# Performance work log

Measured on AMD Instinct MI355X. Metric: run time of the kernel, lower is better.

## Reference

```python
import jax, jax.numpy as jnp
import numpy as np

D_MODEL = 128
D_STATE = 64
EXPAND = 2
D_INNER = EXPAND * D_MODEL  # 256
D_CONV = 4
DT_RANK = (D_MODEL + 15) // 16  # 8
EPS = 1e-6


def setup_inputs() -> dict:
    key = jax.random.key(0)
    ks = jax.random.split(key, 10)
    B, L = 8, 4096
    s = lambda *sh: 1.0 / np.sqrt(sh[-1])
    inp = {
        "x": jax.random.normal(ks[0], (B, L, D_MODEL), jnp.float32),
        "norm_w": jnp.ones((D_MODEL,), jnp.float32),
        "norm_b": jnp.zeros((D_MODEL,), jnp.float32),
        "in_proj_w": jax.random.normal(ks[1], (2 * D_INNER, D_MODEL), jnp.float32) * s(D_MODEL),
        "conv_w": jax.random.normal(ks[2], (D_INNER, 1, D_CONV), jnp.float32) * 0.5,
        "conv_b": jax.random.normal(ks[3], (D_INNER,), jnp.float32) * 0.02,
        "x_proj_w": jax.random.normal(ks[4], (DT_RANK + 2 * D_STATE, D_INNER), jnp.float32) * s(D_INNER),
        "dt_proj_w": jax.random.normal(ks[5], (D_INNER, DT_RANK), jnp.float32) * s(DT_RANK),
        "dt_proj_b": jax.random.uniform(ks[6], (D_INNER,), jnp.float32, -4.0, -2.0),  # softplus -> small dt
        "A_log": jnp.log(jnp.broadcast_to(jnp.arange(1.0, D_STATE + 1.0, dtype=jnp.float32), (D_INNER, D_STATE))),
        "D": jnp.ones((D_INNER,), jnp.float32),
        "out_proj_w": jax.random.normal(ks[7], (D_MODEL, D_INNER), jnp.float32) * s(D_INNER),
    }
    return inp


def _mamba_block(x, norm_w, norm_b, in_proj_w, conv_w, conv_b, x_proj_w,
                 dt_proj_w, dt_proj_b, A_log, Dp, out_proj_w):
    B, L, _ = x.shape
    # LayerNorm (eps=1e-6)
    mu = jnp.mean(x, -1, keepdims=True)
    var = jnp.mean(jnp.square(x - mu), -1, keepdims=True)
    h = (x - mu) * jax.lax.rsqrt(var + EPS) * norm_w + norm_b
    # in_proj -> (u, z), each (B, L, d_inner)
    xz = jnp.einsum('bld,ed->ble', h, in_proj_w)
    u, z = jnp.split(xz, 2, axis=-1)
    # causal depthwise conv1d over L, then SiLU
    u_nch = jnp.transpose(u, (0, 2, 1))  # (B, d_inner, L)
    u_conv = jax.lax.conv_general_dilated(
        u_nch, conv_w, window_strides=(1,), padding=[(D_CONV - 1, 0)],
        feature_group_count=D_INNER, dimension_numbers=('NCH', 'OIH', 'NCH'))
    u_conv = jax.nn.silu(u_conv + conv_b[None, :, None])
    u = jnp.transpose(u_conv, (0, 2, 1))  # (B, L, d_inner)
    # x_proj -> dt, Bmat, Cmat
    x_dbl = jnp.einsum('bld,ed->ble', u, x_proj_w)
    dt, Bmat, Cmat = jnp.split(x_dbl, [DT_RANK, DT_RANK + D_STATE], axis=-1)
    delta = jax.nn.softplus(jnp.einsum('blr,dr->bld', dt, dt_proj_w) + dt_proj_b)  # (B,L,d_inner)
    A = -jnp.exp(A_log)  # (d_inner, d_state)
    # selective scan over L: state (B, d_inner, d_state)
    def step(hS, inp):
        d_t, B_t, C_t, u_t = inp  # (B,dI),(B,N),(B,N),(B,dI)
        dA = jnp.exp(d_t[:, :, None] * A)                      # (B,dI,N)
        hS = dA * hS + (d_t * u_t)[:, :, None] * B_t[:, None, :]
        y = jnp.einsum('bdn,bn->bd', hS, C_t)
        return hS, y
    xs = (jnp.transpose(delta, (1, 0, 2)), jnp.transpose(Bmat, (1, 0, 2)),
          jnp.transpose(Cmat, (1, 0, 2)), jnp.transpose(u, (1, 0, 2)))
    h0 = jnp.zeros((B, D_INNER, D_STATE), x.dtype)
    _, ys = jax.lax.scan(step, h0, xs)
    y = jnp.transpose(ys, (1, 0, 2)) + u * Dp  # (B,L,d_inner)
    y = y * jax.nn.silu(z)
    out = jnp.einsum('bld,ed->ble', y, out_proj_w)  # (B,L,d_model)
    return x + out  # residual (drop_path=0)


def reference(x, norm_w, norm_b, in_proj_w, conv_w, conv_b, x_proj_w,
              dt_proj_w, dt_proj_b, A_log, D, out_proj_w):
    return _mamba_block(x, norm_w, norm_b, in_proj_w, conv_w, conv_b, x_proj_w,
                        dt_proj_w, dt_proj_b, A_log, D, out_proj_w)
```

## Files before the change

kernel.cpp:

```cpp
#include <hip/hip_runtime.h>
#include <math.h>

#define DM 128
#define DI 256
#define DSN 64
#define NB 8
#define LSEQ 4096
#define NTOK (NB*LSEQ)
#define GRP 8
#define GLEN (LSEQ/GRP)

typedef float4 f4;
typedef __attribute__((ext_vector_type(8))) short bf16x8;
typedef __attribute__((ext_vector_type(4))) float f32x4;
typedef __attribute__((ext_vector_type(8))) unsigned short us8;

#if __has_builtin(__builtin_amdgcn_exp2f)
#define EXP2(x) __builtin_amdgcn_exp2f(x)
#else
#define EXP2(x) __expf((x)*0.6931471805599453f)
#endif

__device__ __forceinline__ float sigmoidf_(float x){ return 1.f/(1.f+__expf(-x)); }
__device__ __forceinline__ float rdlane(float v, int j){
    return __int_as_float(__builtin_amdgcn_readlane(__float_as_int(v), j));
}
__device__ __forceinline__ unsigned short f2bf(float f){
    unsigned u = __float_as_uint(f);
    unsigned r = u + 0x7FFFu + ((u>>16)&1u);
    return (unsigned short)(r>>16);
}

__global__ void __launch_bounds__(256) k_lnstats(const float* __restrict__ x, float* __restrict__ stats){
    int tok = blockIdx.x*4 + (threadIdx.x>>6);
    int lane = threadIdx.x & 63;
    const float* row = x + (size_t)tok*DM;
    float a = row[lane], b = row[lane+64];
    float s = a+b, ss = a*a+b*b;
    #pragma unroll
    for (int off=32; off>0; off>>=1){ s += __shfl_xor(s,off); ss += __shfl_xor(ss,off); }
    if (lane==0){
        float mu = s*(1.f/128.f);
        float var = ss*(1.f/128.f) - mu*mu;
        stats[tok*2+0] = mu;
        stats[tok*2+1] = rsqrtf(var + 1e-6f);
    }
}

template<int N_DIM,int K_DIM,int MODE>
__global__ void __launch_bounds__(256) k_gemm_bf(const float* __restrict__ Af32,
    const unsigned short* __restrict__ Abf, const float* __restrict__ Bw,
    float* __restrict__ Cout, float* __restrict__ Cout2, int ldC,
    const float* __restrict__ stats, const float* __restrict__ nw,
    const float* __restrict__ nb, const float* __restrict__ resid)
{
    __shared__ unsigned short Abuf[128*72];
    __shared__ unsigned short Bbuf[64*72];
    const int tid = threadIdx.x;
    const int m0 = blockIdx.x*128;
    const int n0 = blockIdx.y*64;
    const int wave = tid>>6, lane = tid&63;
    const int wm = wave>>1, wn = wave&1;
    const int lr = lane&15, lk = (lane>>4)*8;
    f32x4 acc[4][2];
    #pragma unroll
    for (int i=0;i<4;++i){
        #pragma unroll
        for (int j=0;j<2;++j) acc[i][j] = (f32x4){0.f,0.f,0.f,0.f};
    }

    for (int k0=0; k0<K_DIM; k0+=64){
        {
            int row = tid>>1, ks = (tid&1)*32;
            int m = m0 + row;
            unsigned short* dst = &Abuf[row*72 + ks];
            if (MODE==2){
                const unsigned short* src = Abf + (size_t)m*K_DIM + k0 + ks;
                #pragma unroll
                for (int q=0;q<4;++q) *(us8*)(dst+q*8) = *(const us8*)(src+q*8);
            } else {
                const float* src = Af32 + (size_t)m*K_DIM + k0 + ks;
                float mu=0.f, rs=1.f;
                if (MODE==0){ mu = stats[2*m]; rs = stats[2*m+1]; }
                #pragma unroll
                for (int q=0;q<4;++q){
                    f4 v0 = *(const f4*)(src+q*8);
                    f4 v1 = *(const f4*)(src+q*8+4);
                    if (MODE==0){
                        int kk = k0+ks+q*8;
                        f4 w0=*(const f4*)(nw+kk), w1=*(const f4*)(nw+kk+4);
                        f4 c0=*(const f4*)(nb+kk), c1=*(const f4*)(nb+kk+4);
                        v0.x=(v0.x-mu)*rs*w0.x+c0.x; v0.y=(v0.y-mu)*rs*w0.y+c0.y;
                        v0.z=(v0.z-mu)*rs*w0.z+c0.z; v0.w=(v0.w-mu)*rs*w0.w+c0.w;
                        v1.x=(v1.x-mu)*rs*w1.x+c1.x; v1.y=(v1.y-mu)*rs*w1.y+c1.y;
                        v1.z=(v1.z-mu)*rs*w1.z+c1.z; v1.w=(v1.w-mu)*rs*w1.w+c1.w;
                    }
                    us8 o = {f2bf(v0.x),f2bf(v0.y),f2bf(v0.z),f2bf(v0.w),
                             f2bf(v1.x),f2bf(v1.y),f2bf(v1.z),f2bf(v1.w)};
                    *(us8*)(dst+q*8) = o;
                }
            }
        }
        {
            int row = tid>>2, ks = (tid&3)*16;
            int n = n0 + row;
            unsigned short* dst = &Bbuf[row*72 + ks];
            #pragma unroll
            for (int q=0;q<2;++q){
                f4 v0={0.f,0.f,0.f,0.f}, v1={0.f,0.f,0.f,0.f};
                if (N_DIM%64==0 || n < N_DIM){
                    const float* src = Bw + (size_t)n*K_DIM + k0 + ks + q*8;
                    v0 = *(const f4*)src; v1 = *(const f4*)(src+4);
                }
                us8 o = {f2bf(v0.x),f2bf(v0.y),f2bf(v0.z),f2bf(v0.w),
                         f2bf(v1.x),f2bf(v1.y),f2bf(v1.z),f2bf(v1.w)};
                *(us8*)(dst+q*8) = o;
            }
        }
        __syncthreads();
        #pragma unroll
        for (int kk=0; kk<64; kk+=32){
            bf16x8 bfr[2], afr[4];
            #pragma unroll
            for (int fn=0;fn<2;++fn)
                bfr[fn] = *(const bf16x8*)&Bbuf[(wn*32+fn*16+lr)*72 + kk + lk];
            #pragma unroll
            for (int fm=0;fm<4;++fm)
                afr[fm] = *(const bf16x8*)&Abuf[(wm*64+fm*16+lr)*72 + kk + lk];
            #pragma unroll
            for (int fm=0;fm<4;++fm){
                #pragma unroll
                for (int fn=0;fn<2;++fn)
                    acc[fm][fn] = __builtin_amdgcn_mfma_f32_16x16x32_bf16(afr[fm], bfr[fn], acc[fm][fn], 0,0,0);
            }
        }
        __syncthreads();
    }
    const int cb = (lane>>4)*4;
    #pragma unroll
    for (int fm=0;fm<4;++fm){
        #pragma unroll
        for (int fn=0;fn<2;++fn){
            int col = n0 + wn*32 + fn*16 + lr;
            if (N_DIM%64!=0 && col >= N_DIM) continue;
            #pragma unroll
            for (int r=0;r<4;++r){
                int m = m0 + wm*64 + fm*16 + cb + r;
                float v = acc[fm][fn][r];
                if (MODE==1){
                    if (col < 8) Cout2[(size_t)m*8 + col] = v;
                    else         Cout[(size_t)m*128 + (col-8)] = v;
                } else {
                    if (MODE==2) v += resid[(size_t)m*N_DIM + col];
                    Cout[(size_t)m*ldC + col] = v;
                }
            }
        }
    }
}

__global__ void __launch_bounds__(256) k_trans(const float* __restrict__ ygT,
    const float* __restrict__ xz, unsigned short* __restrict__ ygbf)
{
    __shared__ float T[64][65];
    int t0 = blockIdx.x*64;
    int w  = blockIdx.y;
    int b  = w>>2, d0 = (w&3)*64;
    int tid = threadIdx.x;
    {
        int dl = tid>>2, ts = (tid&3)*16;
        const float* src = ygT + ((size_t)(b*DI + d0 + dl))*LSEQ + t0 + ts;
        #pragma unroll
        for (int q=0;q<4;++q) *(f4*)&T[dl][ts+q*4] = *(const f4*)(src+q*4);
    }
    __syncthreads();
    {
        int tl = tid>>2, ds8 = (tid&3)*16;
        size_t tok = (size_t)(b*LSEQ + t0 + tl);
        const float* zsrc = xz + tok*(2*DI) + DI + d0 + ds8;
        unsigned short* dst = ygbf + tok*DI + d0 + ds8;
        f4 z0 = *(const f4*)zsrc,      z1 = *(const f4*)(zsrc+4);
        f4 z2 = *(const f4*)(zsrc+8),  z3 = *(const f4*)(zsrc+12);
        float zz[16] = {z0.x,z0.y,z0.z,z0.w, z1.x,z1.y,z1.z,z1.w,
                        z2.x,z2.y,z2.z,z2.w, z3.x,z3.y,z3.z,z3.w};
        us8 o0, o1;
        #pragma unroll
        for (int j=0;j<8;++j){
            float g0 = zz[j]   * sigmoidf_(zz[j]);
            float g1 = zz[j+8] * sigmoidf_(zz[j+8]);
            o0[j] = f2bf(T[ds8+j][tl]   * g0);
            o1[j] = f2bf(T[ds8+8+j][tl] * g1);
        }
        *(us8*)dst = o0; *(us8*)(dst+8) = o1;
    }
}

__global__ void __launch_bounds__(256) k_conv(const float* __restrict__ xz,
    const float* __restrict__ cw, const float* __restrict__ cb, float* __restrict__ u)
{
    int idx = blockIdx.x*256 + threadIdx.x;
    int dq = idx & 63;
    int tok = idx >> 6;
    int t = tok & (LSEQ-1);
    f4 w0 = *(const f4*)(cw + (dq*4+0)*4);
    f4 w1 = *(const f4*)(cw + (dq*4+1)*4);
    f4 w2 = *(const f4*)(cw + (dq*4+2)*4);
    f4 w3 = *(const f4*)(cw + (dq*4+3)*4);
    f4 r  = *(const f4*)(cb + dq*4);
    #pragma unroll
    for (int j=0;j<4;++j){
        int tj = t-3+j;
        if (tj < 0) continue;
        f4 v = *(const f4*)(xz + (size_t)(tok-3+j)*(2*DI) + dq*4);
        r.x = fmaf(v.x, ((const float*)&w0)[j], r.x);
        r.y = fmaf(v.y, ((const float*)&w1)[j], r.y);
        r.z = fmaf(v.z, ((const float*)&w2)[j], r.z);
        r.w = fmaf(v.w, ((const float*)&w3)[j], r.w);
    }
    r.x *= sigmoidf_(r.x); r.y *= sigmoidf_(r.y);
    r.z *= sigmoidf_(r.z); r.w *= sigmoidf_(r.w);
    *(f4*)(u + (size_t)tok*DI + dq*4) = r;
}

__global__ void __launch_bounds__(256) k_delta(const float* __restrict__ dt_c,
    const float* __restrict__ Wdt, const float* __restrict__ bdt, float* __restrict__ delta)
{
    int d = threadIdx.x;
    int tok0 = blockIdx.x * 16;
    f4 w0 = *(const f4*)(Wdt + d*8);
    f4 w1 = *(const f4*)(Wdt + d*8 + 4);
    float bias = bdt[d];
    __shared__ float dts[16][8];
    if (threadIdx.x < 128){
        int ti = threadIdx.x >> 3, r = threadIdx.x & 7;
        dts[ti][r] = dt_c[(size_t)(tok0+ti)*8 + r];
    }
    __syncthreads();
    #pragma unroll 4
    for (int ti=0; ti<16; ++ti){
        f4 d0 = *(const f4*)&dts[ti][0];
        f4 d1 = *(const f4*)&dts[ti][4];
        float v = bias;
        v = fmaf(d0.x,w0.x, v); v = fmaf(d0.y,w0.y, v);
        v = fmaf(d0.z,w0.z, v); v = fmaf(d0.w,w0.w, v);
        v = fmaf(d1.x,w1.x, v); v = fmaf(d1.y,w1.y, v);
        v = fmaf(d1.z,w1.z, v); v = fmaf(d1.w,w1.w, v);
        float sp = (v > 20.f) ? v : log1pf(__expf(v));
        delta[(size_t)(tok0+ti)*DI + d] = sp;
    }
}

__global__ void __launch_bounds__(256,8) k_scan1(const float* __restrict__ delta,
    const float* __restrict__ u, const float* __restrict__ bc,
    const float* __restrict__ alog, float* __restrict__ hfin, float* __restrict__ aprod)
{
    int bid = blockIdx.x;
    int b = bid & 7;
    int i = bid >> 3;
    int g = i % 7;
    int dblk = i / 7;
    int wave = threadIdx.x >> 6, lane = threadIdx.x & 63;
    int d = dblk*4 + wave;
    int tok0 = b*LSEQ + g*GLEN;
    const float* dptr = delta + (size_t)tok0*DI + d;
    const float* uptr = u     + (size_t)tok0*DI + d;
    float Acoef = -__expf(alog[d*DSN + lane]) * 1.44269504f;
    float h = 0.f, cum = 0.f;
    float Bpf[8];
    {
        const float* bp = bc + (size_t)tok0*128 + lane;
        #pragma unroll
        for (int k8=0;k8<8;++k8) Bpf[k8] = bp[k8*128];
    }
    const float* bpn = bc + (size_t)(tok0+8)*128 + lane;

    for (int c=0;c<GLEN/64;++c){
        float dv = dptr[(size_t)(c*64+lane)*DI];
        float uv = uptr[(size_t)(c*64+lane)*DI];
        float duv = dv*uv;
        float cs = dv;
        #pragma unroll
        for (int off=32; off; off>>=1) cs += __shfl_xor(cs, off);
        cum += cs;
        #pragma unroll 1
        for (int g8=0;g8<8;++g8){
            #pragma unroll
            for (int k8=0;k8<8;++k8){
                int j = g8*8 + k8;
                float Bn = Bpf[k8];
                Bpf[k8] = bpn[k8*128];
                float sd  = rdlane(dv,  j);
                float sdu = rdlane(duv, j);
                float a = EXP2(Acoef*sd);
                h = fmaf(a, h, sdu*Bn);
            }
            bpn += 8*128;
        }
    }
    size_t idx = ((size_t)(b*DI + d)*GRP + g)*DSN + lane;
    hfin[idx]  = h;
    aprod[idx] = EXP2(Acoef*cum);
}

__global__ void __launch_bounds__(256) k_comb(const float* __restrict__ hfin,
    const float* __restrict__ aprod, float* __restrict__ hin)
{
    int bd = blockIdx.x*4 + (threadIdx.x>>6);
    int lane = threadIdx.x & 63;
    size_t base = (size_t)bd*GRP*DSN + lane;
    float h = 0.f;
    hin[base] = 0.f;
    #pragma unroll
    for (int g=0; g<GRP-1; ++g){
        float hf = hfin[base + (size_t)g*DSN];
        float ap = aprod[base + (size_t)g*DSN];
        h = fmaf(ap, h, hf);
        hin[base + (size_t)(g+1)*DSN] = h;
    }
}

__global__ void __launch_bounds__(256,8) k_scan2(const float* __restrict__ delta,
    const float* __restrict__ u, const float* __restrict__ bc,
    const float* __restrict__ alog, const float* __restrict__ Dp,
    const float* __restrict__ hin, float* __restrict__ ygT)
{
    __shared__ float Q[4][64][17];
    __shared__ float2 DDb[4][64];
    int bid = blockIdx.x;
    int b = bid & 7;
    int i = bid >> 3;
    int g = i & 7;
    int dblk = i >> 3;
    int wave = threadIdx.x >> 6, lane = threadIdx.x & 63;
    int d = dblk*4 + wave;
    int bd = b*DI + d;
    int tok0 = b*LSEQ + g*GLEN;
    float Acoef = -__expf(alog[d*DSN + lane]) * 1.44269504f;
    float Dd = Dp[d];
    float h = hin[((size_t)bd*GRP + g)*DSN + lane];
    const float* dptr = delta + (size_t)tok0*DI + d;
    const float* uptr = u     + (size_t)tok0*DI + d;
    float* yout = ygT + (size_t)bd*LSEQ + g*GLEN;
    float (*Qw)[17] = Q[wave];
    float2* DDw = DDb[wave];
    int q16 = (lane>>4)*16;
    int cidx = lane & 15;
    float Bpf[8], Cpf[8];
    {
        const float* bp = bc + (size_t)tok0*128 + lane;
        #pragma unroll
        for (int k8=0;k8<8;++k8){ Bpf[k8] = bp[k8*128]; Cpf[k8] = bp[k8*128 + 64]; }
    }
    const float* bpn = bc + (size_t)(tok0+8)*128 + lane;

    for (int c=0;c<GLEN/64;++c){
        float dv = dptr[(size_t)(c*64+lane)*DI];
        float uv = uptr[(size_t)(c*64+lane)*DI];
        float duv = dv*uv;
        DDw[lane] = (float2){dv, duv};
        float y = 0.f;
        #pragma unroll 1
        for (int m2=0;m2<4;++m2){
            #pragma unroll 1
            for (int half=0; half<2; ++half){
                #pragma unroll
                for (int k8=0;k8<8;++k8){
                    int j = m2*16 + half*8 + k8;
                    float Bn = Bpf[k8], Cn = Cpf[k8];
                    Bpf[k8] = bpn[k8*128];
                    Cpf[k8] = bpn[k8*128 + 64];
                    float2 sp = DDw[j];
                    float a = EXP2(Acoef*sp.x);
                    h = fmaf(a, h, sp.y*Bn);
                    Qw[lane][half*8+k8] = h*Cn;
                }
                bpn += 8*128;
            }
            float r = 0.f;
            #pragma unroll
            for (int ii=0;ii<16;++ii) r += Qw[q16+ii][cidx];
            r += __shfl_xor(r, 16);
            r += __shfl_xor(r, 32);
            y = ((lane>>4)==m2) ? r : y;
        }
        yout[c*64 + lane] = fmaf(uv, Dd, y);
    }
}

extern "C" void kernel_launch(void* const* d_in, const int* in_sizes, int n_in,
                              void* d_out, int out_size, void* d_ws, size_t ws_size,
                              hipStream_t stream)
{
    (void)in_sizes; (void)n_in; (void)out_size; (void)ws_size;
    const float* x    = (const float*)d_in[0];
    const float* nw   = (const float*)d_in[1];
    const float* nb   = (const float*)d_in[2];
    const float* w_in = (const float*)d_in[3];
    const float* cw   = (const float*)d_in[4];
    const float* cb   = (const float*)d_in[5];
    const float* wx   = (const float*)d_in[6];
    const float* wdt  = (const float*)d_in[7];
    const float* bdt  = (const float*)d_in[8];
    const float* alog = (const float*)d_in[9];
    const float* Dp   = (const float*)d_in[10];
    const float* wo   = (const float*)d_in[11];
    float* out = (float*)d_out;

    float* ws    = (float*)d_ws;
    float* xz    = ws;
    float* u     = xz    + (size_t)NTOK*2*DI;
    float* bcp   = u     + (size_t)NTOK*DI;
    float* dt_c  = bcp   + (size_t)NTOK*128 + 2048;
    float* delta = dt_c  + (size_t)NTOK*8;
    float* ygT   = delta + (size_t)NTOK*DI;
    float* stats = ygT   + (size_t)NTOK*DI;
    float* hfin  = stats + (size_t)NTOK*2;
    float* aprod = hfin  + (size_t)NB*DI*GRP*DSN;
    float* hin   = aprod + (size_t)NB*DI*GRP*DSN;
    unsigned short* ygbf = (unsigned short*)(hin + (size_t)NB*DI*GRP*DSN);

    k_lnstats<<<NTOK/4, 256, 0, stream>>>(x, stats);

    dim3 g1(NTOK/128, 512/64);
    k_gemm_bf<512,128,0><<<g1, 256, 0, stream>>>(x, nullptr, w_in, xz, nullptr, 512, stats, nw, nb, nullptr);

    k_conv<<<NTOK*64/256, 256, 0, stream>>>(xz, cw, cb, u);

    dim3 g2(NTOK/128, 3);
    k_gemm_bf<136,256,1><<<g2, 256, 0, stream>>>(u, nullptr, wx, bcp, dt_c, 0, nullptr, nullptr, nullptr, nullptr);

    k_delta<<<NTOK/16, 256, 0, stream>>>(dt_c, wdt, bdt, delta);

    k_scan1<<<NB*(GRP-1)*64, 256, 0, stream>>>(delta, u, bcp, alog, hfin, aprod);
    k_comb<<<NB*DI/4, 256, 0, stream>>>(hfin, aprod, hin);
    k_scan2<<<NB*GRP*64, 256, 0, stream>>>(delta, u, bcp, alog, Dp, hin, ygT);

    dim3 gt(LSEQ/64, NB*4);
    k_trans<<<gt, 256, 0, stream>>>(ygT, xz, ygbf);

    dim3 g3(NTOK/128, 2);
    k_gemm_bf<128,256,2><<<g3, 256, 0, stream>>>(nullptr, ygbf, wo, out, nullptr, 128, nullptr, nullptr, nullptr, x);
}
```

Before: 479.2 us.

## Interleave B/C and delta/delta*u buffers, move D-skip into transpose kernel

The x_proj GEMM epilogue now writes B and C interleaved per state, plus a separate B-only array for the first scan pass. The delta kernel writes (delta, delta*u) pairs so both scans issue one float2 load instead of two strided loads. The scan1 kernel replaces readlane broadcasts with an LDS buffer, and the u*D skip term moves from scan2 into the transpose/gating kernel. The aim is fewer scattered global loads and less ALU work in the scan hot loops, at the cost of extra writes for the duplicate B array and the wider delta buffer.

```diff
diff --git a/kernel.cpp b/kernel.cpp
--- a/kernel.cpp
+++ b/kernel.cpp
@@ -22,9 +22,6 @@
 #endif
 
 __device__ __forceinline__ float sigmoidf_(float x){ return 1.f/(1.f+__expf(-x)); }
-__device__ __forceinline__ float rdlane(float v, int j){
-    return __int_as_float(__builtin_amdgcn_readlane(__float_as_int(v), j));
-}
 __device__ __forceinline__ unsigned short f2bf(float f){
     unsigned u = __float_as_uint(f);
     unsigned r = u + 0x7FFFu + ((u>>16)&1u);
@@ -50,8 +47,8 @@
 template<int N_DIM,int K_DIM,int MODE>
 __global__ void __launch_bounds__(256) k_gemm_bf(const float* __restrict__ Af32,
     const unsigned short* __restrict__ Abf, const float* __restrict__ Bw,
-    float* __restrict__ Cout, float* __restrict__ Cout2, int ldC,
-    const float* __restrict__ stats, const float* __restrict__ nw,
+    float* __restrict__ Cout, float* __restrict__ Cout2, float* __restrict__ Cout3,
+    int ldC, const float* __restrict__ stats, const float* __restrict__ nw,
     const float* __restrict__ nb, const float* __restrict__ resid)
 {
     __shared__ unsigned short Abuf[128*72];
@@ -149,7 +146,14 @@
                 float v = acc[fm][fn][r];
                 if (MODE==1){
                     if (col < 8) Cout2[(size_t)m*8 + col] = v;
-                    else         Cout[(size_t)m*128 + (col-8)] = v;
+                    else if (col < 72){
+                        int n = col - 8;
+                        Cout[(size_t)m*128 + 2*n] = v;
+                        Cout3[(size_t)m*64 + n] = v;
+                    } else {
+                        int n = col - 72;
+                        Cout[(size_t)m*128 + 2*n + 1] = v;
+                    }
                 } else {
                     if (MODE==2) v += resid[(size_t)m*N_DIM + col];
                     Cout[(size_t)m*ldC + col] = v;
@@ -160,7 +164,8 @@
 }
 
 __global__ void __launch_bounds__(256) k_trans(const float* __restrict__ ygT,
-    const float* __restrict__ xz, unsigned short* __restrict__ ygbf)
+    const float* __restrict__ xz, const float* __restrict__ u,
+    const float* __restrict__ Dp, unsigned short* __restrict__ ygbf)
 {
     __shared__ float T[64][65];
     int t0 = blockIdx.x*64;
@@ -178,18 +183,31 @@
         int tl = tid>>2, ds8 = (tid&3)*16;
         size_t tok = (size_t)(b*LSEQ + t0 + tl);
         const float* zsrc = xz + tok*(2*DI) + DI + d0 + ds8;
+        const float* usrc = u  + tok*DI + d0 + ds8;
         unsigned short* dst = ygbf + tok*DI + d0 + ds8;
         f4 z0 = *(const f4*)zsrc,      z1 = *(const f4*)(zsrc+4);
         f4 z2 = *(const f4*)(zsrc+8),  z3 = *(const f4*)(zsrc+12);
+        f4 u0 = *(const f4*)usrc,      u1 = *(const f4*)(usrc+4);
+        f4 u2 = *(const f4*)(usrc+8),  u3 = *(const f4*)(usrc+12);
+        f4 D0 = *(const f4*)(Dp+d0+ds8);
+        f4 D1 = *(const f4*)(Dp+d0+ds8+4);
+        f4 D2 = *(const f4*)(Dp+d0+ds8+8);
+        f4 D3 = *(const f4*)(Dp+d0+ds8+12);
         float zz[16] = {z0.x,z0.y,z0.z,z0.w, z1.x,z1.y,z1.z,z1.w,
                         z2.x,z2.y,z2.z,z2.w, z3.x,z3.y,z3.z,z3.w};
+        float uu[16] = {u0.x,u0.y,u0.z,u0.w, u1.x,u1.y,u1.z,u1.w,
+                        u2.x,u2.y,u2.z,u2.w, u3.x,u3.y,u3.z,u3.w};
+        float DD[16] = {D0.x,D0.y,D0.z,D0.w, D1.x,D1.y,D1.z,D1.w,
+                        D2.x,D2.y,D2.z,D2.w, D3.x,D3.y,D3.z,D3.w};
         us8 o0, o1;
         #pragma unroll
         for (int j=0;j<8;++j){
             float g0 = zz[j]   * sigmoidf_(zz[j]);
             float g1 = zz[j+8] * sigmoidf_(zz[j+8]);
-            o0[j] = f2bf(T[ds8+j][tl]   * g0);
-            o1[j] = f2bf(T[ds8+8+j][tl] * g1);
+            float y0 = fmaf(DD[j],   uu[j],   T[ds8+j][tl]);
+            float y1 = fmaf(DD[j+8], uu[j+8], T[ds8+8+j][tl]);
+            o0[j] = f2bf(y0 * g0);
+            o1[j] = f2bf(y1 * g1);
         }
         *(us8*)dst = o0; *(us8*)(dst+8) = o1;
     }
@@ -223,7 +241,8 @@
 }
 
 __global__ void __launch_bounds__(256) k_delta(const float* __restrict__ dt_c,
-    const float* __restrict__ Wdt, const float* __restrict__ bdt, float* __restrict__ delta)
+    const float* __restrict__ u, const float* __restrict__ Wdt,
+    const float* __restrict__ bdt, float* __restrict__ dd2)
 {
     int d = threadIdx.x;
     int tok0 = blockIdx.x * 16;
@@ -246,14 +265,16 @@
         v = fmaf(d1.x,w1.x, v); v = fmaf(d1.y,w1.y, v);
         v = fmaf(d1.z,w1.z, v); v = fmaf(d1.w,w1.w, v);
         float sp = (v > 20.f) ? v : log1pf(__expf(v));
-        delta[(size_t)(tok0+ti)*DI + d] = sp;
-    }
-}
-
-__global__ void __launch_bounds__(256,8) k_scan1(const float* __restrict__ delta,
-    const float* __restrict__ u, const float* __restrict__ bc,
-    const float* __restrict__ alog, float* __restrict__ hfin, float* __restrict__ aprod)
-{
+        float uv = u[(size_t)(tok0+ti)*DI + d];
+        *(float2*)&dd2[(size_t)(tok0+ti)*2*DI + 2*d] = (float2){sp, sp*uv};
+    }
+}
+
+__global__ void __launch_bounds__(256,8) k_scan1(const float* __restrict__ dd2,
+    const float* __restrict__ bs, const float* __restrict__ alog,
+    float* __restrict__ hfin, float* __restrict__ aprod)
+{
+    __shared__ float2 DDb[4][64];
     int bid = blockIdx.x;
     int b = bid & 7;
     int i = bid >> 3;
@@ -262,23 +283,22 @@
     int wave = threadIdx.x >> 6, lane = threadIdx.x & 63;
     int d = dblk*4 + wave;
     int tok0 = b*LSEQ + g*GLEN;
-    const float* dptr = delta + (size_t)tok0*DI + d;
-    const float* uptr = u     + (size_t)tok0*DI + d;
+    const float* ddp = dd2 + (size_t)tok0*2*DI + 2*d;
     float Acoef = -__expf(alog[d*DSN + lane]) * 1.44269504f;
     float h = 0.f, cum = 0.f;
+    float2* DDw = DDb[wave];
     float Bpf[8];
     {
-        const float* bp = bc + (size_t)tok0*128 + lane;
-        #pragma unroll
-        for (int k8=0;k8<8;++k8) Bpf[k8] = bp[k8*128];
-    }
-    const float* bpn = bc + (size_t)(tok0+8)*128 + lane;
+        const float* bp = bs + (size_t)tok0*64 + lane;
+        #pragma unroll
+        for (int k8=0;k8<8;++k8) Bpf[k8] = bp[k8*64];
+    }
+    const float* bpn = bs + (size_t)(tok0+8)*64 + lane;
 
     for (int c=0;c<GLEN/64;++c){
-        float dv = dptr[(size_t)(c*64+lane)*DI];
-        float uv = uptr[(size_t)(c*64+lane)*DI];
-        float duv = dv*uv;
-        float cs = dv;
+        float2 dd = *(const float2*)&ddp[(size_t)(c*64+lane)*2*DI];
+        DDw[lane] = dd;
+        float cs = dd.x;
         #pragma unroll
         for (int off=32; off; off>>=1) cs += __shfl_xor(cs, off);
         cum += cs;
@@ -288,13 +308,12 @@
             for (int k8=0;k8<8;++k8){
                 int j = g8*8 + k8;
                 float Bn = Bpf[k8];
-                Bpf[k8] = bpn[k8*128];
-                float sd  = rdlane(dv,  j);
-                float sdu = rdlane(duv, j);
-                float a = EXP2(Acoef*sd);
-                h = fmaf(a, h, sdu*Bn);
-            }
-            bpn += 8*128;
+                Bpf[k8] = bpn[k8*64];
+                float2 sp = DDw[j];
+                float a = EXP2(Acoef*sp.x);
+                h = fmaf(a, h, sp.y*Bn);
+            }
+            bpn += 8*64;
         }
     }
     size_t idx = ((size_t)(b*DI + d)*GRP + g)*DSN + lane;
@@ -319,9 +338,8 @@
     }
 }
 
-__global__ void __launch_bounds__(256,8) k_scan2(const float* __restrict__ delta,
-    const float* __restrict__ u, const float* __restrict__ bc,
-    const float* __restrict__ alog, const float* __restrict__ Dp,
+__global__ void __launch_bounds__(256,8) k_scan2(const float* __restrict__ dd2,
+    const float* __restrict__ bci, const float* __restrict__ alog,
     const float* __restrict__ hin, float* __restrict__ ygT)
 {
     __shared__ float Q[4][64][17];
@@ -336,28 +354,24 @@
     int bd = b*DI + d;
     int tok0 = b*LSEQ + g*GLEN;
     float Acoef = -__expf(alog[d*DSN + lane]) * 1.44269504f;
-    float Dd = Dp[d];
     float h = hin[((size_t)bd*GRP + g)*DSN + lane];
-    const float* dptr = delta + (size_t)tok0*DI + d;
-    const float* uptr = u     + (size_t)tok0*DI + d;
+    const float* ddp = dd2 + (size_t)tok0*2*DI + 2*d;
     float* yout = ygT + (size_t)bd*LSEQ + g*GLEN;
     float (*Qw)[17] = Q[wave];
     float2* DDw = DDb[wave];
     int q16 = (lane>>4)*16;
     int cidx = lane & 15;
-    float Bpf[8], Cpf[8];
+    float2 BC[8];
     {
-        const float* bp = bc + (size_t)tok0*128 + lane;
-        #pragma unroll
-        for (int k8=0;k8<8;++k8){ Bpf[k8] = bp[k8*128]; Cpf[k8] = bp[k8*128 + 64]; }
-    }
-    const float* bpn = bc + (size_t)(tok0+8)*128 + lane;
+        const float* bp = bci + (size_t)tok0*128 + 2*lane;
+        #pragma unroll
+        for (int k8=0;k8<8;++k8) BC[k8] = *(const float2*)&bp[k8*128];
+    }
+    const float* bpn = bci + (size_t)(tok0+8)*128 + 2*lane;
 
     for (int c=0;c<GLEN/64;++c){
-        float dv = dptr[(size_t)(c*64+lane)*DI];
-        float uv = uptr[(size_t)(c*64+lane)*DI];
-        float duv = dv*uv;
-        DDw[lane] = (float2){dv, duv};
+        float2 dd = *(const float2*)&ddp[(size_t)(c*64+lane)*2*DI];
+        DDw[lane] = dd;
         float y = 0.f;
         #pragma unroll 1
         for (int m2=0;m2<4;++m2){
@@ -366,13 +380,12 @@
                 #pragma unroll
                 for (int k8=0;k8<8;++k8){
                     int j = m2*16 + half*8 + k8;
-                    float Bn = Bpf[k8], Cn = Cpf[k8];
-                    Bpf[k8] = bpn[k8*128];
-                    Cpf[k8] = bpn[k8*128 + 64];
+                    float2 bcv = BC[k8];
+                    BC[k8] = *(const float2*)&bpn[k8*128];
                     float2 sp = DDw[j];
                     float a = EXP2(Acoef*sp.x);
-                    h = fmaf(a, h, sp.y*Bn);
-                    Qw[lane][half*8+k8] = h*Cn;
+                    h = fmaf(a, h, sp.y*bcv.x);
+                    Qw[lane][half*8+k8] = h*bcv.y;
                 }
                 bpn += 8*128;
             }
@@ -383,7 +396,7 @@
             r += __shfl_xor(r, 32);
             y = ((lane>>4)==m2) ? r : y;
         }
-        yout[c*64 + lane] = fmaf(uv, Dd, y);
+        yout[c*64 + lane] = y;
     }
 }
 
@@ -409,10 +422,11 @@
     float* ws    = (float*)d_ws;
     float* xz    = ws;
     float* u     = xz    + (size_t)NTOK*2*DI;
-    float* bcp   = u     + (size_t)NTOK*DI;
-    float* dt_c  = bcp   + (size_t)NTOK*128 + 2048;
-    float* delta = dt_c  + (size_t)NTOK*8;
-    float* ygT   = delta + (size_t)NTOK*DI;
+    float* bci   = u     + (size_t)NTOK*DI;
+    float* bcs1  = bci   + (size_t)NTOK*128;
+    float* dt_c  = bcs1  + (size_t)NTOK*64;
+    float* dd2   = dt_c  + (size_t)NTOK*8;
+    float* ygT   = dd2   + (size_t)NTOK*2*DI;
     float* stats = ygT   + (size_t)NTOK*DI;
     float* hfin  = stats + (size_t)NTOK*2;
     float* aprod = hfin  + (size_t)NB*DI*GRP*DSN;
@@ -422,22 +436,22 @@
     k_lnstats<<<NTOK/4, 256, 0, stream>>>(x, stats);
 
     dim3 g1(NTOK/128, 512/64);
-    k_gemm_bf<512,128,0><<<g1, 256, 0, stream>>>(x, nullptr, w_in, xz, nullptr, 512, stats, nw, nb, nullptr);
+    k_gemm_bf<512,128,0><<<g1, 256, 0, stream>>>(x, nullptr, w_in, xz, nullptr, nullptr, 512, stats, nw, nb, nullptr);
 
     k_conv<<<NTOK*64/256, 256, 0, stream>>>(xz, cw, cb, u);
 
     dim3 g2(NTOK/128, 3);
-    k_gemm_bf<136,256,1><<<g2, 256, 0, stream>>>(u, nullptr, wx, bcp, dt_c, 0, nullptr, nullptr, nullptr, nullptr);
-
-    k_delta<<<NTOK/16, 256, 0, stream>>>(dt_c, wdt, bdt, delta);
-
-    k_scan1<<<NB*(GRP-1)*64, 256, 0, stream>>>(delta, u, bcp, alog, hfin, aprod);
+    k_gemm_bf<136,256,1><<<g2, 256, 0, stream>>>(u, nullptr, wx, bci, dt_c, bcs1, 0, nullptr, nullptr, nullptr, nullptr);
+
+    k_delta<<<NTOK/16, 256, 0, stream>>>(dt_c, u, wdt, bdt, dd2);
+
+    k_scan1<<<NB*(GRP-1)*64, 256, 0, stream>>>(dd2, bcs1, alog, hfin, aprod);
     k_comb<<<NB*DI/4, 256, 0, stream>>>(hfin, aprod, hin);
-    k_scan2<<<NB*GRP*64, 256, 0, stream>>>(delta, u, bcp, alog, Dp, hin, ygT);
+    k_scan2<<<NB*GRP*64, 256, 0, stream>>>(dd2, bci, alog, hin, ygT);
 
     dim3 gt(LSEQ/64, NB*4);
-    k_trans<<<gt, 256, 0, stream>>>(ygT, xz, ygbf);
+    k_trans<<<gt, 256, 0, stream>>>(ygT, xz, u, Dp, ygbf);
 
     dim3 g3(NTOK/128, 2);
-    k_gemm_bf<128,256,2><<<g3, 256, 0, stream>>>(nullptr, ygbf, wo, out, nullptr, 128, nullptr, nullptr, nullptr, x);
-}
+    k_gemm_bf<128,256,2><<<g3, 256, 0, stream>>>(nullptr, ygbf, wo, out, nullptr, nullptr, 128, nullptr, nullptr, nullptr, x);
+}
```

After: 507.4 us. +5.9%, slower.
